# Kernel tuning notes

Measured on AMD Instinct MI355X. Metric: run time of the kernel, lower is better.

Reference implementation:

```python
import jax, jax.numpy as jnp
import numpy as np

B, T, C, Q, NW, MD = 4, 2048, 512, 300, 32, 256
WS, NC, S = 16, 4, 16
L = T - WS + 1  # unfold output length, stride 1, no pad


def _pe(x):
    # standard sinusoidal positional encoding added to x [B,t,d]
    t, d = x.shape[1], x.shape[2]
    pos = jnp.arange(t, dtype=jnp.float32)[:, None]
    div = jnp.exp(jnp.arange(0, d, 2, dtype=jnp.float32) * (-np.log(10000.0) / d))
    ang = pos * div                                   # [t, d//2]
    pe = jnp.stack([jnp.sin(ang), jnp.cos(ang)], axis=-1).reshape(t, d)
    return x + pe[None]


def _mlp(x, w1, b1, w2, b2):
    return jax.nn.relu(x @ w1 + b1) @ w2 + b2


def setup_inputs():
    key = jax.random.key(0)
    ks = iter(jax.random.split(key, 32))

    def lin(k, fin, fout):
        kw, kb = jax.random.split(k)
        return (jax.random.normal(kw, (fin, fout), jnp.float32) / np.sqrt(fin),
                jax.random.normal(kb, (fout,), jnp.float32) * 0.01)

    inp = {}
    inp["vis_feats"] = jax.random.normal(next(ks), (B, T, C), jnp.float32)
    inp["query_feats"] = jax.random.normal(next(ks), (B, NW, Q), jnp.float32)
    inp["vW1"], inp["vb1"] = lin(next(ks), C, C)
    inp["vW2"], inp["vb2"] = lin(next(ks), C, C)
    inp["s1W1"], inp["s1b1"] = lin(next(ks), Q, Q)
    inp["s1W2"], inp["s1b2"] = lin(next(ks), Q, C)
    inp["s2W1"], inp["s2b1"] = lin(next(ks), Q, Q)
    inp["s2W2"], inp["s2b2"] = lin(next(ks), Q, C)
    inp["pW1"], inp["pb1"] = lin(next(ks), NC * C, C)
    inp["pW2"], inp["pb2"] = lin(next(ks), C, 2)
    inp["mW"], inp["mb"] = lin(next(ks), C, MD)
    inp["stW"], inp["stb"] = lin(next(ks), MD * S, S)
    inp["enW"], inp["enb"] = lin(next(ks), MD * S, S)
    inp["vis_len"] = jax.random.randint(next(ks), (B,), L // 2, L + 1, dtype=jnp.int32)
    return inp


def reference(vis_feats, query_feats, vW1, vb1, vW2, vb2,
              s1W1, s1b1, s1W2, s1b2, s2W1, s2b1, s2W2, s2b2,
              pW1, pb1, pW2, pb2, mW, mb, stW, stb, enW, enb, vis_len):
    v = _mlp(_pe(vis_feats), vW1, vb1, vW2, vb2)                # [B,T,C]
    q = _pe(query_feats)
    enc1 = _mlp(q, s1W1, s1b1, s1W2, s1b2)                      # [B,NW,C]
    enc2 = _mlp(q, s2W1, s2b1, s2W2, s2b2)                      # [B,NW,C]
    sim = jnp.einsum('btc,bwc->btw', v, enc1)                   # [B,T,NW]

    widx = jnp.arange(L)[:, None] + jnp.arange(WS)[None, :]     # [L,WS] sliding windows
    vu = v[:, widx, :].reshape(B, L, NC, WS // NC, C).mean(axis=3)       # [B,L,NC,C] avg-pool per chunk
    bel = sim[:, widx, :].reshape(B, L, NC, WS // NC, NW).sum(axis=3)    # [B,L,NC,NW]
    labels = jnp.argmax(bel, axis=3)                            # [B,L,NC] selected word per chunk
    sel = jax.vmap(lambda e, lab: e[lab])(enc2, labels)         # [B,L,NC,C] gather word embeddings
    mod = sel * vu                                              # modulate

    pred = _mlp(mod.reshape(B, L, NC * C), pW1, pb1, pW2, pb2).transpose(0, 2, 1)  # [B,2,L]

    x = (mod @ mW + mb).reshape(B, L * NC, MD)                  # [B,N,MD]
    n = (vis_len * NC).astype(jnp.int32)                        # ragged valid length per batch
    i = jnp.arange(S, dtype=jnp.int32)
    starts = (n[:, None] * i[None, :]) // S                     # adaptive-maxpool bin bounds
    ends = (n[:, None] * (i[None, :] + 1) + S - 1) // S
    j = jnp.arange(L * NC, dtype=jnp.int32)
    cols = []
    for b in range(S):  # S is a small fixed constant (not a data dim)
        m = (j[None, :] >= starts[:, b:b + 1]) & (j[None, :] < ends[:, b:b + 1])  # [B,N]
        cols.append(jnp.max(jnp.where(m[:, :, None], x, -jnp.inf), axis=1))       # [B,MD]
    feat = jnp.stack(cols, axis=2).reshape(B, MD * S)           # [B,MD,S] flattened channel-major
    start = (feat @ stW + stb)[:, :, None]                      # [B,S,1]
    end = (feat @ enW + enb)[:, :, None]                        # [B,S,1]
    return pred, start, end
```

## Files before the change

### kernel.cpp

```cpp
#include <hip/hip_runtime.h>
#include <hip/hip_bf16.h>
#include <math.h>

#define BB 4
#define TT 2048
#define CC 512
#define QQ 300
#define NWW 32
#define MDD 256
#define WSS 16
#define NCC 4
#define SS 16
#define LL (TT - WSS + 1)
#define NSUB 8
#define PUL (TT - 3)

typedef __attribute__((ext_vector_type(8))) short short8;
typedef __attribute__((ext_vector_type(4))) short short4v;
typedef __attribute__((ext_vector_type(4))) float f32x4;

__device__ __forceinline__ void pe_add4(f32x4& v, int t, int gk0)
{
    #pragma unroll
    for (int j = 0; j < 4; j++) {
        int gk = gk0 + j;
        float di = expf((float)(gk & ~1) * (-9.210340371976184f / (float)CC));
        float ang = (float)t * di;
        v[j] += (gk & 1) ? cosf(ang) : sinf(ang);
    }
}

template<int PE>
__global__ __launch_bounds__(256, 2) void gemm_f32_fast(
    const float* __restrict__ A, const float* __restrict__ Bm,
    const float* __restrict__ bias, float* __restrict__ Cm,
    int M, int N, int K, int do_relu)
{
    __shared__ float As[2][32][68];
    __shared__ float Bs[2][32][128];
    const int bm = blockIdx.x * 64;
    const int bn = blockIdx.y * 128;
    const int tid = threadIdx.x;
    const int tx = tid & 31;
    const int ty = tid >> 5;

    float acc[8][4] = {};
    f32x4 pa[2], pb[4];
    int am[2], akq[2], bkr[4], bnq[4];
    #pragma unroll
    for (int i = 0; i < 2; i++) {
        int idx = i * 256 + tid;
        am[i] = idx >> 3; akq[i] = (idx & 7) * 4;
    }
    #pragma unroll
    for (int i = 0; i < 4; i++) {
        int idx = i * 256 + tid;
        bkr[i] = idx >> 5; bnq[i] = (idx & 31) * 4;
    }

    const int nk0 = K / 32;
    #pragma unroll
    for (int i = 0; i < 2; i++) {
        pa[i] = *(const f32x4*)(A + (size_t)(bm + am[i]) * K + akq[i]);
        if (PE) pe_add4(pa[i], (bm + am[i]) & (TT - 1), akq[i]);
    }
    #pragma unroll
    for (int i = 0; i < 4; i++)
        pb[i] = *(const f32x4*)(Bm + (size_t)bkr[i] * N + bn + bnq[i]);

    int buf = 0;
    for (int k0i = 0; ; k0i++) {
        #pragma unroll
        for (int i = 0; i < 2; i++)
            #pragma unroll
            for (int j = 0; j < 4; j++) As[buf][akq[i] + j][am[i]] = pa[i][j];
        #pragma unroll
        for (int i = 0; i < 4; i++)
            *(f32x4*)&Bs[buf][bkr[i]][bnq[i]] = pb[i];
        __syncthreads();
        if (k0i + 1 < nk0) {
            int k0 = (k0i + 1) * 32;
            #pragma unroll
            for (int i = 0; i < 2; i++) {
                pa[i] = *(const f32x4*)(A + (size_t)(bm + am[i]) * K + k0 + akq[i]);
                if (PE) pe_add4(pa[i], (bm + am[i]) & (TT - 1), k0 + akq[i]);
            }
            #pragma unroll
            for (int i = 0; i < 4; i++)
                pb[i] = *(const f32x4*)(Bm + (size_t)(k0 + bkr[i]) * N + bn + bnq[i]);
        }
        #pragma unroll 8
        for (int kk = 0; kk < 32; kk++) {
            f32x4 a0 = *(const f32x4*)&As[buf][kk][ty * 8];
            f32x4 a1 = *(const f32x4*)&As[buf][kk][ty * 8 + 4];
            f32x4 b0 = *(const f32x4*)&Bs[buf][kk][tx * 4];
            #pragma unroll
            for (int i2 = 0; i2 < 4; i2++)
                #pragma unroll
                for (int j2 = 0; j2 < 4; j2++) {
                    acc[i2][j2]     += a0[i2] * b0[j2];
                    acc[i2 + 4][j2] += a1[i2] * b0[j2];
                }
        }
        buf ^= 1;
        if (k0i + 1 == nk0) break;
    }

    #pragma unroll
    for (int i = 0; i < 8; i++) {
        int gm = bm + ty * 8 + i;
        f32x4 o;
        #pragma unroll
        for (int j = 0; j < 4; j++) {
            float v0 = acc[i][j] + bias[bn + tx * 4 + j];
            if (do_relu) v0 = fmaxf(v0, 0.f);
            o[j] = v0;
        }
        *(f32x4*)(Cm + (size_t)gm * N + bn + tx * 4) = o;
    }
}

__global__ void qpe_kernel(const float* __restrict__ q, float* __restrict__ out)
{
    int idx = blockIdx.x * 256 + threadIdx.x;
    if (idx >= BB * NWW * QQ) return;
    int qi = idx % QQ;
    int w  = (idx / QQ) % NWW;
    float di = expf((float)(qi & ~1) * (-9.210340371976184f / (float)QQ));
    float ang = (float)w * di;
    out[idx] = q[idx] + ((qi & 1) ? cosf(ang) : sinf(ang));
}

__global__ __launch_bounds__(64) void sgemm_dual2(
    const float* __restrict__ A1, const float* __restrict__ W1,
    const float* __restrict__ b1, float* __restrict__ C1,
    const float* __restrict__ A2, const float* __restrict__ W2,
    const float* __restrict__ b2, float* __restrict__ C2,
    int M, int N, int K, int do_relu)
{
    int id = blockIdx.x * 64 + threadIdx.x;
    if (id >= M * N) return;
    const float* A = blockIdx.y ? A2 : A1;
    const float* B = blockIdx.y ? W2 : W1;
    const float* bias = blockIdx.y ? b2 : b1;
    float* C = blockIdx.y ? C2 : C1;
    int m = id / N, n = id % N;
    const float* a = A + (size_t)m * K;
    const float* b = B + n;
    float acc = 0.f;
    int k = 0;
    for (; k + 10 <= K; k += 10) {
        float av[10], bv[10];
        #pragma unroll
        for (int u = 0; u < 10; u++) av[u] = a[k + u];
        #pragma unroll
        for (int u = 0; u < 10; u++) bv[u] = b[(size_t)(k + u) * N];
        #pragma unroll
        for (int u = 0; u < 10; u++) acc = fmaf(av[u], bv[u], acc);
    }
    for (; k < K; k++) acc = fmaf(a[k], b[(size_t)k * N], acc);
    float val = acc + bias[n];
    if (do_relu) val = fmaxf(val, 0.f);
    C[id] = val;
}

template<int PARTIAL>
__global__ __launch_bounds__(256) void gemm_bf16_k64(
    const short* __restrict__ A, int lda,
    const short* __restrict__ Bt, int ldb,
    const float* __restrict__ bias, float* __restrict__ C,
    int M, int N, int Kp, int do_relu)
{
    __shared__ short As[128][72];
    __shared__ short Bs[128][72];
    const int bm = blockIdx.x * 128;
    const int bn = blockIdx.y * 128;
    const int kbase = PARTIAL ? blockIdx.z * Kp : 0;
    float* Cout = PARTIAL ? C + (size_t)blockIdx.z * ((size_t)M * N) : C;
    const int tid = threadIdx.x;
    const int wave = tid >> 6, lane = tid & 63;
    const int wm = (wave & 1) * 64, wn = (wave >> 1) * 64;
    const int l15 = lane & 15;
    const int lk0 = (lane >> 4) * 8;
    const int srow = tid >> 3;
    const int scol = (tid & 7) * 8;

    f32x4 acc[4][4] = {};

    for (int k0 = kbase; k0 < kbase + Kp; k0 += 64) {
        #pragma unroll
        for (int p = 0; p < 4; p++) {
            int row = p * 32 + srow;
            short8 av = {};
            int gm = bm + row;
            if (gm < M) av = *(const short8*)(A + (size_t)gm * lda + k0 + scol);
            *(short8*)&As[row][scol] = av;
            short8 bv = {};
            int gn = bn + row;
            if (gn < N) bv = *(const short8*)(Bt + (size_t)gn * ldb + k0 + scol);
            *(short8*)&Bs[row][scol] = bv;
        }
        __syncthreads();

        #pragma unroll
        for (int ks = 0; ks < 2; ks++) {
            int lk = lk0 + ks * 32;
            short8 af[4], bf[4];
            #pragma unroll
            for (int mi = 0; mi < 4; mi++)
                af[mi] = *(const short8*)&As[wm + mi * 16 + l15][lk];
            #pragma unroll
            for (int ni = 0; ni < 4; ni++)
                bf[ni] = *(const short8*)&Bs[wn + ni * 16 + l15][lk];
            #pragma unroll
            for (int mi = 0; mi < 4; mi++)
                #pragma unroll
                for (int ni = 0; ni < 4; ni++)
                    acc[mi][ni] = __builtin_amdgcn_mfma_f32_16x16x32_bf16(
                        af[mi], bf[ni], acc[mi][ni], 0, 0, 0);
        }
        __syncthreads();
    }

    #pragma unroll
    for (int mi = 0; mi < 4; mi++) {
        int row0 = bm + wm + mi * 16 + (lane >> 4) * 4;
        #pragma unroll
        for (int ni = 0; ni < 4; ni++) {
            int col = bn + wn + ni * 16 + l15;
            float bsv = (!PARTIAL && bias) ? bias[col] : 0.f;
            #pragma unroll
            for (int r = 0; r < 4; r++) {
                int grow = row0 + r;
                if (grow >= M) continue;
                float val = acc[mi][ni][r] + bsv;
                if (!PARTIAL && do_relu) val = fmaxf(val, 0.f);
                Cout[(size_t)grow * N + col] = val;
            }
        }
    }
}

__global__ __launch_bounds__(256) void convT2_kernel(
    const float* __restrict__ src, __hip_bfloat16* __restrict__ dst,
    int K, int N)
{
    __shared__ float t[32][33];
    int c = threadIdx.x & 31, r4 = threadIdx.x >> 5;
    int n0 = blockIdx.x * 32, k0 = blockIdx.y * 32;
    #pragma unroll
    for (int rr = 0; rr < 32; rr += 8)
        t[rr + r4][c] = src[(size_t)(k0 + rr + r4) * N + n0 + c];
    __syncthreads();
    #pragma unroll
    for (int rr = 0; rr < 32; rr += 8)
        dst[(size_t)(n0 + rr + r4) * K + k0 + c] = __float2bfloat16(t[c][rr + r4]);
}

__global__ __launch_bounds__(256) void sim_kernel(
    const float* __restrict__ v, const float* __restrict__ enc1,
    float* __restrict__ sim)
{
    __shared__ float vs[16][CC];
    int blk = blockIdx.x;
    int b  = blk / (TT / 16);
    int t0 = (blk % (TT / 16)) * 16;
    int tid = threadIdx.x;
    for (int i = tid; i < 16 * (CC / 4); i += 256) {
        int r = i / (CC / 4), c = i % (CC / 4);
        *(f32x4*)&vs[r][c * 4] =
            *(const f32x4*)(v + ((size_t)b * TT + t0 + r) * CC + c * 4);
    }
    __syncthreads();
    int w  = tid & 31;
    int tt = (tid >> 5) * 2;
    const f32x4* e4 = (const f32x4*)(enc1 + ((size_t)b * NWW + w) * CC);
    const f32x4* va = (const f32x4*)vs[tt];
    const f32x4* vb = (const f32x4*)vs[tt + 1];
    float s0 = 0.f, s1 = 0.f;
    #pragma unroll 4
    for (int kq = 0; kq < CC / 4; kq++) {
        f32x4 ee = e4[kq];
        f32x4 aa = va[kq], bb = vb[kq];
        s0 = fmaf(aa[0], ee[0], s0);
        s0 = fmaf(aa[1], ee[1], s0);
        s0 = fmaf(aa[2], ee[2], s0);
        s0 = fmaf(aa[3], ee[3], s0);
        s1 = fmaf(bb[0], ee[0], s1);
        s1 = fmaf(bb[1], ee[1], s1);
        s1 = fmaf(bb[2], ee[2], s1);
        s1 = fmaf(bb[3], ee[3], s1);
    }
    sim[((size_t)b * TT + t0 + tt) * NWW + w] = s0;
    sim[((size_t)b * TT + t0 + tt + 1) * NWW + w] = s1;
}

__global__ __launch_bounds__(256) void pu_kernel(
    const float* __restrict__ v, float* __restrict__ pu)
{
    int idx = blockIdx.x * 256 + threadIdx.x;
    if (idx >= BB * PUL * (CC / 4)) return;
    int q = idx % (CC / 4);
    int t = (idx / (CC / 4)) % PUL;
    int b = idx / ((CC / 4) * PUL);
    const float* vp = v + ((size_t)b * TT + t) * CC + q * 4;
    f32x4 r0 = *(const f32x4*)vp;
    f32x4 r1 = *(const f32x4*)(vp + CC);
    f32x4 r2 = *(const f32x4*)(vp + 2 * CC);
    f32x4 r3 = *(const f32x4*)(vp + 3 * CC);
    f32x4 o;
    #pragma unroll
    for (int j = 0; j < 4; j++)
        o[j] = 0.25f * (((r0[j] + r1[j]) + r2[j]) + r3[j]);
    *(f32x4*)(pu + ((size_t)b * PUL + t) * CC + q * 4) = o;
}

__global__ __launch_bounds__(256) void mod_kernel(
    const float* __restrict__ pu, const float* __restrict__ sim,
    const float* __restrict__ enc2, __hip_bfloat16* __restrict__ modb)
{
    int blk = blockIdx.x;
    int b = blk / LL, l = blk % LL;
    int tid = threadIdx.x;
    int cch = tid >> 6;
    int lane = tid & 63;
    int t0 = l + cch * 4;

    int w = lane & 31;
    const float* sp = sim + ((size_t)b * TT + t0) * NWW + w;
    float bel = sp[0] + sp[NWW] + sp[2 * NWW] + sp[3 * NWW];
    int idx = w;
    #pragma unroll
    for (int m = 1; m < 32; m <<= 1) {
        float ov = __shfl_xor(bel, m);
        int   oi = __shfl_xor(idx, m);
        if (ov > bel || (ov == bel && oi < idx)) { bel = ov; idx = oi; }
    }

    const f32x4* e2 = (const f32x4*)(enc2 + ((size_t)b * NWW + idx) * CC);
    const f32x4* pq = (const f32x4*)(pu + ((size_t)b * PUL + t0) * CC);
    __hip_bfloat16* mp = modb + (((size_t)blk) * NCC + cch) * CC;
    #pragma unroll
    for (int q = lane; q < CC / 4; q += 64) {
        f32x4 e = e2[q], p = pq[q];
        short4v o;
        #pragma unroll
        for (int j = 0; j < 4; j++) {
            __hip_bfloat16 h = __float2bfloat16(e[j] * p[j]);
            o[j] = *(short*)&h;
        }
        *(short4v*)(mp + q * 4) = o;
    }
}

__global__ __launch_bounds__(256) void pred2w_fused(
    const float* __restrict__ p,
    const float* __restrict__ pb1,
    const float* __restrict__ pW2, const float* __restrict__ pb2,
    float* __restrict__ out)
{
    const int ML = BB * LL;
    int row = blockIdx.x * 4 + (threadIdx.x >> 6);
    if (row >= ML) return;
    int lane = threadIdx.x & 63;
    size_t off = (size_t)row * CC + lane * 8;
    f32x4 a0 = *(const f32x4*)(p + off);
    f32x4 a1 = *(const f32x4*)(p + off + 4);
    f32x4 c0 = *(const f32x4*)(p + (size_t)ML * CC + off);
    f32x4 c1 = *(const f32x4*)(p + (size_t)ML * CC + off + 4);
    f32x4 bb0 = *(const f32x4*)(pb1 + lane * 8);
    f32x4 bb1 = *(const f32x4*)(pb1 + lane * 8 + 4);
    f32x4 h0, h1;
    #pragma unroll
    for (int j = 0; j < 4; j++) {
        h0[j] = fmaxf(a0[j] + c0[j] + bb0[j], 0.f);
        h1[j] = fmaxf(a1[j] + c1[j] + bb1[j], 0.f);
    }
    const float* wp = pW2 + lane * 16;
    f32x4 w0 = *(const f32x4*)wp;
    f32x4 w1 = *(const f32x4*)(wp + 4);
    f32x4 w2 = *(const f32x4*)(wp + 8);
    f32x4 w3 = *(const f32x4*)(wp + 12);
    float s0 = h0[0]*w0[0] + h0[1]*w0[2] + h0[2]*w1[0] + h0[3]*w1[2]
             + h1[0]*w2[0] + h1[1]*w2[2] + h1[2]*w3[0] + h1[3]*w3[2];
    float s1 = h0[0]*w0[1] + h0[1]*w0[3] + h0[2]*w1[1] + h0[3]*w1[3]
             + h1[0]*w2[1] + h1[1]*w2[3] + h1[2]*w3[1] + h1[3]*w3[3];
    #pragma unroll
    for (int m = 32; m; m >>= 1) {
        s0 += __shfl_xor(s0, m);
        s1 += __shfl_xor(s1, m);
    }
    if (lane == 0) {
        int b = row / LL, l = row % LL;
        out[((size_t)b * 2 + 0) * LL + l] = s0 + pb2[0];
        out[((size_t)b * 2 + 1) * LL + l] = s1 + pb2[1];
    }
}

__global__ __launch_bounds__(256) void pool1_kernel(
    const float* __restrict__ x, const int* __restrict__ vis_len,
    float* __restrict__ scratch)
{
    int blk = blockIdx.x;
    int sub = blk % NSUB;
    int s   = (blk / NSUB) % SS;
    int b   = blk / (NSUB * SS);
    int n = vis_len[b] * NCC;
    int st = (n * s) / SS;
    int en = (n * (s + 1) + SS - 1) / SS;
    int len = en - st;
    int j0 = st + (len * sub) / NSUB;
    int j1 = st + (len * (sub + 1)) / NSUB;
    int md = threadIdx.x;
    float m = -INFINITY;
    const float* xp = x + (size_t)b * (LL * NCC) * MDD + md;
    for (int j = j0; j < j1; j++) m = fmaxf(m, xp[(size_t)j * MDD]);
    scratch[(size_t)blk * MDD + md] = m;
}

__global__ __launch_bounds__(256) void pool2_kernel(
    const float* __restrict__ scratch, float* __restrict__ feat)
{
    int blk = blockIdx.x;
    int md = threadIdx.x;
    const float* sp = scratch + (size_t)blk * NSUB * MDD + md;
    float m = sp[0];
    #pragma unroll
    for (int i = 1; i < NSUB; i++) m = fmaxf(m, sp[(size_t)i * MDD]);
    int b = blk / SS, s = blk % SS;
    feat[(size_t)b * MDD * SS + md * SS + s] = m;
}

__global__ void stend_kernel(const float* __restrict__ feat,
                             const float* __restrict__ stW, const float* __restrict__ stb,
                             const float* __restrict__ enW, const float* __restrict__ enb,
                             float* __restrict__ out)
{
    int bid = blockIdx.x;
    int which = bid >> 6;
    int r = bid & 63;
    int b = r >> 4, s = r & 15;
    int lane = threadIdx.x;
    const float* W  = which ? enW : stW;
    const float* bb = which ? enb : stb;
    const float* f  = feat + (size_t)b * MDD * SS;
    float acc = 0.f;
    for (int k = lane; k < MDD * SS; k += 64) acc += f[k] * W[(size_t)k * SS + s];
    #pragma unroll
    for (int m = 32; m; m >>= 1) acc += __shfl_xor(acc, m);
    if (lane == 0)
        out[(size_t)BB * 2 * LL + which * (BB * SS) + b * SS + s] = acc + bb[s];
}

extern "C" void kernel_launch(void* const* d_in, const int* in_sizes, int n_in,
                              void* d_out, int out_size, void* d_ws, size_t ws_size,
                              hipStream_t stream)
{
    const float* vis  = (const float*)d_in[0];
    const float* qf   = (const float*)d_in[1];
    const float* vW1  = (const float*)d_in[2];  const float* vb1 = (const float*)d_in[3];
    const float* vW2  = (const float*)d_in[4];  const float* vb2 = (const float*)d_in[5];
    const float* s1W1 = (const float*)d_in[6];  const float* s1b1= (const float*)d_in[7];
    const float* s1W2 = (const float*)d_in[8];  const float* s1b2= (const float*)d_in[9];
    const float* s2W1 = (const float*)d_in[10]; const float* s2b1= (const float*)d_in[11];
    const float* s2W2 = (const float*)d_in[12]; const float* s2b2= (const float*)d_in[13];
    const float* pW1  = (const float*)d_in[14]; const float* pb1 = (const float*)d_in[15];
    const float* pW2  = (const float*)d_in[16]; const float* pb2 = (const float*)d_in[17];
    const float* mW   = (const float*)d_in[18]; const float* mb  = (const float*)d_in[19];
    const float* stW  = (const float*)d_in[20]; const float* stb = (const float*)d_in[21];
    const float* enW  = (const float*)d_in[22]; const float* enb = (const float*)d_in[23];
    const int*   vlen = (const int*)d_in[24];
    float* out = (float*)d_out;

    float* ws   = (float*)d_ws;
    float* h1   = ws;
    float* v    = h1   + (size_t)BB * TT * CC;
    float* qpe  = v    + (size_t)BB * TT * CC;
    float* qh   = qpe  + (size_t)BB * NWW * QQ;
    float* enc1 = qh   + (size_t)BB * NWW * QQ;
    float* enc2 = enc1 + (size_t)BB * NWW * CC;
    float* sim  = enc2 + (size_t)BB * NWW * CC;
    float* feat = sim  + (size_t)BB * TT * NWW;
    float* x    = feat + (size_t)BB * MDD * SS;
    float* fend = x    + (size_t)BB * LL * NCC * MDD;
    __hip_bfloat16* modb = (__hip_bfloat16*)fend;
    __hip_bfloat16* pW1t = modb + (size_t)BB * LL * NCC * CC;
    __hip_bfloat16* mWt  = pW1t + (size_t)CC * (NCC * CC);
    float* qh2 = (float*)(mWt + (size_t)CC * MDD);

    const int MT = BB * TT;
    const int ML = BB * LL;
    const int MX = BB * LL * NCC;

    convT2_kernel<<<dim3(CC / 32, (NCC * CC) / 32), 256, 0, stream>>>(pW1, pW1t, NCC * CC, CC);
    convT2_kernel<<<dim3(MDD / 32, CC / 32), 256, 0, stream>>>(mW, mWt, CC, MDD);

    gemm_f32_fast<1><<<dim3(MT / 64, CC / 128), 256, 0, stream>>>(
        vis, vW1, vb1, h1, MT, CC, CC, 1);
    gemm_f32_fast<0><<<dim3(MT / 64, CC / 128), 256, 0, stream>>>(
        h1, vW2, vb2, v, MT, CC, CC, 0);
    qpe_kernel<<<(BB * NWW * QQ + 255) / 256, 256, 0, stream>>>(qf, qpe);
    sgemm_dual2<<<dim3((BB * NWW * QQ + 63) / 64, 2), 64, 0, stream>>>(
        qpe, s1W1, s1b1, qh, qpe, s2W1, s2b1, qh2, BB * NWW, QQ, QQ, 1);
    sgemm_dual2<<<dim3((BB * NWW * CC + 63) / 64, 2), 64, 0, stream>>>(
        qh, s1W2, s1b2, enc1, qh2, s2W2, s2b2, enc2, BB * NWW, CC, QQ, 0);
    sim_kernel<<<BB * (TT / 16), 256, 0, stream>>>(v, enc1, sim);
    pu_kernel<<<(BB * PUL * (CC / 4) + 255) / 256, 256, 0, stream>>>(v, h1);
    mod_kernel<<<BB * LL, 256, 0, stream>>>(h1, sim, enc2, modb);
    gemm_bf16_k64<1><<<dim3(ML / 128 + 1, CC / 128, 2), 256, 0, stream>>>(
        (const short*)modb, NCC * CC, (const short*)pW1t, NCC * CC,
        nullptr, x, ML, CC, (NCC * CC) / 2, 0);
    pred2w_fused<<<(ML + 3) / 4, 256, 0, stream>>>(x, pb1, pW2, pb2, out);
    gemm_bf16_k64<0><<<dim3((MX + 127) / 128, MDD / 128), 256, 0, stream>>>(
        (const short*)modb, CC, (const short*)mWt, CC, mb, x, MX, MDD, CC, 0);
    pool1_kernel<<<BB * SS * NSUB, 256, 0, stream>>>(x, vlen, sim);
    pool2_kernel<<<BB * SS, 256, 0, stream>>>(sim, feat);
    stend_kernel<<<128, 64, 0, stream>>>(feat, stW, stb, enW, enb, out);
}
```

Before: 360.9 us.

## Skip pooled-away GEMM tiles past vis_len, store pooling input as bf16

The mW GEMM now returns early for 128-row tiles that lie entirely beyond the valid length vis_len*NC of their batch, because adaptive max-pooling never reads those rows. Its output is written as bf16 instead of fp32, which halves the store and pool-read traffic. The two weight-transpose launches are merged into one kernel. Rounding the pooled values to bf16 adds precision loss, though pooling was already fed bf16-computed GEMM results.

Measured after the change: 359.3 us. Within noise of the previous version (-0.5%).

```diff
diff --git a/kernel.cpp b/kernel.cpp
--- a/kernel.cpp
+++ b/kernel.cpp
@@ -164,17 +164,28 @@
     C[id] = val;
 }
 
-template<int PARTIAL>
+template<int PARTIAL, int OUT16, int SKIP>
 __global__ __launch_bounds__(256) void gemm_bf16_k64(
     const short* __restrict__ A, int lda,
     const short* __restrict__ Bt, int ldb,
     const float* __restrict__ bias, float* __restrict__ C,
+    __hip_bfloat16* __restrict__ C16, const int* __restrict__ vlen,
     int M, int N, int Kp, int do_relu)
 {
     __shared__ short As[128][72];
     __shared__ short Bs[128][72];
     const int bm = blockIdx.x * 128;
     const int bn = blockIdx.y * 128;
+
+    if (SKIP) {
+        int b0 = bm / (LL * NCC);
+        int rib = bm - b0 * (LL * NCC);
+        int last = bm + 127 < M - 1 ? bm + 127 : M - 1;
+        int b1 = last / (LL * NCC);
+        bool valid = (rib < vlen[b0] * NCC) || (b1 != b0);
+        if (!valid) return;
+    }
+
     const int kbase = PARTIAL ? blockIdx.z * Kp : 0;
     float* Cout = PARTIAL ? C + (size_t)blockIdx.z * ((size_t)M * N) : C;
     const int tid = threadIdx.x;
@@ -235,19 +246,32 @@
                 if (grow >= M) continue;
                 float val = acc[mi][ni][r] + bsv;
                 if (!PARTIAL && do_relu) val = fmaxf(val, 0.f);
-                Cout[(size_t)grow * N + col] = val;
+                if (OUT16)
+                    C16[(size_t)grow * N + col] = __float2bfloat16(val);
+                else
+                    Cout[(size_t)grow * N + col] = val;
             }
         }
     }
 }
 
-__global__ __launch_bounds__(256) void convT2_kernel(
-    const float* __restrict__ src, __hip_bfloat16* __restrict__ dst,
-    int K, int N)
+__global__ __launch_bounds__(256) void convT2_dual(
+    const float* __restrict__ pW1, __hip_bfloat16* __restrict__ pW1t,
+    const float* __restrict__ mW, __hip_bfloat16* __restrict__ mWt)
 {
     __shared__ float t[32][33];
     int c = threadIdx.x & 31, r4 = threadIdx.x >> 5;
-    int n0 = blockIdx.x * 32, k0 = blockIdx.y * 32;
+    const float* src; __hip_bfloat16* dst;
+    int K, N, n0, k0;
+    int id = blockIdx.x;
+    if (id < 1024) {
+        src = pW1; dst = pW1t; K = NCC * CC; N = CC;
+        n0 = (id & 15) * 32; k0 = (id >> 4) * 32;
+    } else {
+        id -= 1024;
+        src = mW; dst = mWt; K = CC; N = MDD;
+        n0 = (id & 7) * 32; k0 = (id >> 3) * 32;
+    }
     #pragma unroll
     for (int rr = 0; rr < 32; rr += 8)
         t[rr + r4][c] = src[(size_t)(k0 + rr + r4) * N + n0 + c];
@@ -398,7 +422,7 @@
 }
 
 __global__ __launch_bounds__(256) void pool1_kernel(
-    const float* __restrict__ x, const int* __restrict__ vis_len,
+    const __hip_bfloat16* __restrict__ x, const int* __restrict__ vis_len,
     float* __restrict__ scratch)
 {
     int blk = blockIdx.x;
@@ -413,8 +437,9 @@
     int j1 = st + (len * (sub + 1)) / NSUB;
     int md = threadIdx.x;
     float m = -INFINITY;
-    const float* xp = x + (size_t)b * (LL * NCC) * MDD + md;
-    for (int j = j0; j < j1; j++) m = fmaxf(m, xp[(size_t)j * MDD]);
+    const __hip_bfloat16* xp = x + (size_t)b * (LL * NCC) * MDD + md;
+    for (int j = j0; j < j1; j++)
+        m = fmaxf(m, __bfloat162float(xp[(size_t)j * MDD]));
     scratch[(size_t)blk * MDD + md] = m;
 }
 
@@ -487,13 +512,13 @@
     __hip_bfloat16* pW1t = modb + (size_t)BB * LL * NCC * CC;
     __hip_bfloat16* mWt  = pW1t + (size_t)CC * (NCC * CC);
     float* qh2 = (float*)(mWt + (size_t)CC * MDD);
+    __hip_bfloat16* xb16 = (__hip_bfloat16*)x;
 
     const int MT = BB * TT;
     const int ML = BB * LL;
     const int MX = BB * LL * NCC;
 
-    convT2_kernel<<<dim3(CC / 32, (NCC * CC) / 32), 256, 0, stream>>>(pW1, pW1t, NCC * CC, CC);
-    convT2_kernel<<<dim3(MDD / 32, CC / 32), 256, 0, stream>>>(mW, mWt, CC, MDD);
+    convT2_dual<<<1152, 256, 0, stream>>>(pW1, pW1t, mW, mWt);
 
     gemm_f32_fast<1><<<dim3(MT / 64, CC / 128), 256, 0, stream>>>(
         vis, vW1, vb1, h1, MT, CC, CC, 1);
@@ -507,13 +532,14 @@
     sim_kernel<<<BB * (TT / 16), 256, 0, stream>>>(v, enc1, sim);
     pu_kernel<<<(BB * PUL * (CC / 4) + 255) / 256, 256, 0, stream>>>(v, h1);
     mod_kernel<<<BB * LL, 256, 0, stream>>>(h1, sim, enc2, modb);
-    gemm_bf16_k64<1><<<dim3(ML / 128 + 1, CC / 128, 2), 256, 0, stream>>>(
+    gemm_bf16_k64<1, 0, 0><<<dim3(ML / 128 + 1, CC / 128, 2), 256, 0, stream>>>(
         (const short*)modb, NCC * CC, (const short*)pW1t, NCC * CC,
-        nullptr, x, ML, CC, (NCC * CC) / 2, 0);
+        nullptr, x, nullptr, nullptr, ML, CC, (NCC * CC) / 2, 0);
     pred2w_fused<<<(ML + 3) / 4, 256, 0, stream>>>(x, pb1, pW2, pb2, out);
-    gemm_bf16_k64<0><<<dim3((MX + 127) / 128, MDD / 128), 256, 0, stream>>>(
-        (const short*)modb, CC, (const short*)mWt, CC, mb, x, MX, MDD, CC, 0);
-    pool1_kernel<<<BB * SS * NSUB, 256, 0, stream>>>(x, vlen, sim);
+    gemm_bf16_k64<0, 1, 1><<<dim3((MX + 127) / 128, MDD / 128), 256, 0, stream>>>(
+        (const short*)modb, CC, (const short*)mWt, CC, mb, nullptr, xb16, vlen,
+        MX, MDD, CC, 0);
+    pool1_kernel<<<BB * SS * NSUB, 256, 0, stream>>>(xb16, vlen, sim);
     pool2_kernel<<<BB * SS, 256, 0, stream>>>(sim, feat);
     stend_kernel<<<128, 64, 0, stream>>>(feat, stW, stb, enW, enb, out);
 }
```
